# Kernel tuning notes

Hardware: AMD Instinct MI355X
Metric: run time of the kernel (lower is better)

Reference implementation:

```python
import jax, jax.numpy as jnp
import numpy as np

B, N, D, H = 4, 2048, 512, 8
HD = D // H
NUM_BUCKETS, MAX_EXACT, MAX_DIST = 44, 28, 2048
_BAND_RANGES = [range(38, 44), range(34, 40), range(28, 35), range(20, 28),
                range(13, 21), range(7, 14), range(3, 9), range(0, 6)]


def _band_mask():
    m = np.zeros((NUM_BUCKETS, H), dtype=np.float32)
    for h, band in enumerate(_BAND_RANGES):
        for j in band:
            m[j, h] = 1.0
    return jnp.asarray(m)


def _rel_bucket(n):
    # T5-style causal relative-position buckets: exact for d<MAX_EXACT, log-spaced above.
    i = jnp.arange(n)[:, None]
    j = jnp.arange(n)[None, :]
    d = jnp.maximum(i - j, 0)
    safe = jnp.maximum(d, 1).astype(jnp.float32)
    logb = MAX_EXACT + (jnp.log(safe / MAX_EXACT)
                        / np.log(MAX_DIST / MAX_EXACT)
                        * (NUM_BUCKETS - MAX_EXACT)).astype(jnp.int32)
    return jnp.where(d < MAX_EXACT, d, jnp.minimum(logb, NUM_BUCKETS - 1))  # [n,n]


def setup_inputs() -> dict:
    key = jax.random.key(0)
    ks = jax.random.split(key, 12)
    s = 0.02
    return {
        "x": jax.random.normal(ks[0], (B, N, D), jnp.float32),
        "k_delta": jax.random.normal(ks[1], (B, H, N, HD), jnp.float32) * 0.1,
        "v_delta": jax.random.normal(ks[2], (B, H, N, HD), jnp.float32) * 0.1,
        "qkv_w": jax.random.normal(ks[3], (D, 3 * D), jnp.float32) * s,
        "qkv_b": jnp.zeros((3 * D,), jnp.float32),
        "gate_w": jax.random.normal(ks[4], (D, D), jnp.float32) * s,
        "gate_b": jnp.zeros((D,), jnp.float32),
        "out_w": jax.random.normal(ks[5], (D, D), jnp.float32) * s,
        "out_b": jnp.zeros((D,), jnp.float32),
        "pos_bias": jax.random.normal(ks[6], (NUM_BUCKETS, H), jnp.float32) * 0.1,
        "if_gain": jnp.ones((H,), jnp.float32),
    }


def reference(x, k_delta, v_delta, qkv_w, qkv_b, gate_w, gate_b,
              out_w, out_b, pos_bias, if_gain):
    b, n, d = x.shape
    band = _band_mask()
    # hard per-head banding of the relative bias
    eff_bias = pos_bias * band + (1.0 - band) * (-100.0)           # [44,H]
    qkv = x @ qkv_w + qkv_b                                         # [B,N,3D]
    q, k, v = jnp.split(qkv, 3, axis=-1)
    q = q.reshape(b, n, H, HD).transpose(0, 2, 1, 3)                # [B,H,N,HD]
    k = k.reshape(b, n, H, HD).transpose(0, 2, 1, 3) + k_delta
    v = v.reshape(b, n, H, HD).transpose(0, 2, 1, 3) + v_delta
    bucket = _rel_bucket(n)                                         # [N,N] int
    bias = eff_bias[bucket].transpose(2, 0, 1)                      # [H,N,N]
    scores = jnp.einsum("bhid,bhjd->bhij", q, k) / np.sqrt(HD) + bias[None]
    causal = jnp.tril(jnp.ones((n, n), bool))
    scores = jnp.where(causal[None, None], scores, -1e9)
    attn = jax.nn.softmax(scores, axis=-1)
    out = jnp.einsum("bhij,bhjd->bhid", attn, v)                    # [B,H,N,HD]
    out = out * if_gain[None, :, None, None]                        # IF gain
    out_flat = out.transpose(0, 2, 1, 3).reshape(b, n, d)
    gate = jax.nn.sigmoid(x @ gate_w + gate_b)                      # output gating
    return (out_flat * gate) @ out_w + out_b
```

## Files before the change

kernel.cpp:

```cpp
#include <hip/hip_runtime.h>
#include <cmath>

typedef unsigned short u16;
typedef unsigned short u16x4 __attribute__((ext_vector_type(4)));
typedef unsigned short u16x8 __attribute__((ext_vector_type(8)));
typedef __bf16 bf16x8 __attribute__((ext_vector_type(8)));
typedef float f32x4 __attribute__((ext_vector_type(4)));

#define HNUM 8
#define HDIM 64
#define BATCH 4
#define NSEQ 2048
#define DMODEL 512
#define NFUSED 2048
#define LP 72
#define CP 132

__device__ __forceinline__ u16 f2bf(float f) {
  unsigned int u = __builtin_bit_cast(unsigned int, f);
  u += 0x7fffu + ((u >> 16) & 1u);
  return (u16)(u >> 16);
}

__device__ __forceinline__ float bf2f(u16 v) {
  unsigned int u = ((unsigned int)v) << 16;
  return __builtin_bit_cast(float, u);
}

__device__ __forceinline__ f32x4 mfma_bf16(u16x8 a, u16x8 b, f32x4 c) {
  return __builtin_amdgcn_mfma_f32_16x16x32_bf16(
      __builtin_bit_cast(bf16x8, a), __builtin_bit_cast(bf16x8, b), c, 0, 0, 0);
}

__device__ __forceinline__ void gload16(u16* lds, const u16* g) {
  __builtin_amdgcn_global_load_lds(
      (const __attribute__((address_space(1))) void*)g,
      (__attribute__((address_space(3))) void*)lds, 16, 0, 0);
}

template <int ROWS>
__device__ __forceinline__ void stage_tile(u16* lds, const u16* g, int tid) {
  #pragma unroll
  for (int i = 0; i < ROWS / 64; ++i) {
    const int off = (i * 256 + tid) * 8;
    const int row = off >> 5, col = off & 31;
    gload16(lds + off, g + (size_t)row * DMODEL + col);
  }
}

__global__ __launch_bounds__(256) void cvt_bf16_kernel(
    const float* __restrict__ in, u16* __restrict__ out, int n8) {
  int i = blockIdx.x * 256 + threadIdx.x;
  if (i >= n8) return;
  const float4 f0 = *(const float4*)(in + i * 8);
  const float4 f1 = *(const float4*)(in + i * 8 + 4);
  u16x8 pk;
  pk[0] = f2bf(f0.x); pk[1] = f2bf(f0.y); pk[2] = f2bf(f0.z); pk[3] = f2bf(f0.w);
  pk[4] = f2bf(f1.x); pk[5] = f2bf(f1.y); pk[6] = f2bf(f1.z); pk[7] = f2bf(f1.w);
  *(u16x8*)(out + i * 8) = pk;
}

__global__ __launch_bounds__(256) void transpose_w_kernel(
    const float* __restrict__ W, u16* __restrict__ Wt, int K, int N) {
  __shared__ float tile[32][33];
  const int n0 = blockIdx.x * 32, k0 = blockIdx.y * 32;
  const int tx = threadIdx.x & 31, ty = threadIdx.x >> 5;
  #pragma unroll
  for (int yy = ty; yy < 32; yy += 8)
    tile[yy][tx] = W[(size_t)(k0 + yy) * N + n0 + tx];
  __syncthreads();
  #pragma unroll
  for (int yy = ty; yy < 32; yy += 8)
    Wt[(size_t)(n0 + yy) * K + k0 + tx] = f2bf(tile[tx][yy]);
}

__global__ __launch_bounds__(256) void transpose_v_kernel(
    const u16* __restrict__ v, u16* __restrict__ vT) {
  __shared__ u16 t[64][LP];
  const int n0 = blockIdx.x * 64;
  const size_t bh = blockIdx.y;
  const int r = threadIdx.x >> 2, c0 = (threadIdx.x & 3) << 4;
  const u16* src = v + (bh * NSEQ + n0 + r) * HDIM + c0;
  u16x8 a0 = *(const u16x8*)src;
  u16x8 a1 = *(const u16x8*)(src + 8);
  #pragma unroll
  for (int j = 0; j < 8; ++j) {
    t[c0 + j][r] = a0[j];
    t[c0 + 8 + j][r] = a1[j];
  }
  __syncthreads();
  u16x8 o0 = *(const u16x8*)&t[r][c0];
  u16x8 o1 = *(const u16x8*)&t[r][c0 + 8];
  u16* dst = vT + (bh * HDIM + r) * NSEQ + n0 + c0;
  *(u16x8*)dst = o0;
  *(u16x8*)(dst + 8) = o1;
}

__global__ __launch_bounds__(256) void bias_tab_kernel(
    const float* __restrict__ pos_bias, float* __restrict__ tab) {
  int d = blockIdx.x * 256 + threadIdx.x;
  if (d >= NSEQ) return;
  int bkt;
  if (d < 28) {
    bkt = d;
  } else {
    double t = log((double)d / 28.0) / log(2048.0 / 28.0) * 16.0;
    int ti = 28 + (int)t;
    bkt = ti < 43 ? ti : 43;
  }
  const int lo[8] = {38, 34, 28, 20, 13, 7, 3, 0};
  const int hi[8] = {44, 40, 35, 28, 21, 14, 9, 6};
  #pragma unroll
  for (int h = 0; h < HNUM; ++h) {
    bool inb = (bkt >= lo[h]) && (bkt < hi[h]);
    tab[h * NSEQ + d] = inb ? pos_bias[bkt * HNUM + h] : -100.0f;
  }
}

__global__ __launch_bounds__(256) void gemm_fused(
    const u16* __restrict__ Abf, const u16* __restrict__ Wt,
    const float* __restrict__ qkv_b, const float* __restrict__ gate_b,
    const float* __restrict__ kdelta, const float* __restrict__ vdelta,
    u16* __restrict__ qbf, u16* __restrict__ kbf, u16* __restrict__ vbf,
    u16* __restrict__ gate) {
  __shared__ __align__(16) u16 S[6][128 * 32];

  const int bid = blockIdx.y * 16 + blockIdx.x;
  const int nb = (bid & 7) * 128 + (bid >> 3);
  const int m0 = (nb >> 4) * 128;
  const int n0 = (nb & 15) * 128;

  const int tid = threadIdx.x;
  const int w = tid >> 6, l = tid & 63, li = l & 15, lg = l >> 4;
  const int wr = w >> 1, wc = w & 1;

  f32x4 acc[4][4];
  #pragma unroll
  for (int i = 0; i < 4; ++i)
    #pragma unroll
    for (int j = 0; j < 4; ++j) acc[i][j] = f32x4{0.f, 0.f, 0.f, 0.f};

  const u16* Ab = Abf + (size_t)m0 * DMODEL;
  const u16* Bb = Wt + (size_t)n0 * DMODEL;

  stage_tile<128>(S[0], Ab, tid);
  stage_tile<128>(S[3], Bb, tid);
  stage_tile<128>(S[1], Ab + 32, tid);
  stage_tile<128>(S[4], Bb + 32, tid);

  #pragma unroll
  for (int kt = 0; kt < 16; ++kt) {
    if (kt + 2 < 16) {
      stage_tile<128>(S[(kt + 2) % 3], Ab + (kt + 2) * 32, tid);
      stage_tile<128>(S[3 + (kt + 2) % 3], Bb + (kt + 2) * 32, tid);
    }
    if (kt < 14)       asm volatile("s_waitcnt vmcnt(8)" ::: "memory");
    else if (kt == 14) asm volatile("s_waitcnt vmcnt(4)" ::: "memory");
    else               asm volatile("s_waitcnt vmcnt(0)" ::: "memory");
    __builtin_amdgcn_s_barrier();
    __builtin_amdgcn_sched_barrier(0);
    const u16* Asb = S[kt % 3];
    const u16* Bsb = S[3 + kt % 3];
    u16x8 af[4], bfr[4];
    #pragma unroll
    for (int mt = 0; mt < 4; ++mt)
      af[mt] = *(const u16x8*)&Asb[(wr * 64 + mt * 16 + li) * 32 + lg * 8];
    #pragma unroll
    for (int nt = 0; nt < 4; ++nt)
      bfr[nt] = *(const u16x8*)&Bsb[(wc * 64 + nt * 16 + li) * 32 + lg * 8];
    asm volatile("s_waitcnt lgkmcnt(0)" ::: "memory");
    __builtin_amdgcn_sched_barrier(0);
    #pragma unroll
    for (int mt = 0; mt < 4; ++mt)
      #pragma unroll
      for (int nt = 0; nt < 4; ++nt)
        acc[mt][nt] = mfma_bf16(af[mt], bfr[nt], acc[mt][nt]);
    __builtin_amdgcn_s_barrier();
    __builtin_amdgcn_sched_barrier(0);
  }

  u16* Ct = S[0];
  const int seg = n0 >> 9;
  #pragma unroll
  for (int nt = 0; nt < 4; ++nt) {
    const int col = wc * 64 + nt * 16 + li;
    const int colg = n0 + col;
    const float bv = (seg < 3) ? qkv_b[colg] : gate_b[colg & 511];
    #pragma unroll
    for (int mt = 0; mt < 4; ++mt) {
      const int row = wr * 64 + mt * 16 + lg * 4;
      #pragma unroll
      for (int r = 0; r < 4; ++r)
        Ct[(row + r) * CP + col] = f2bf(acc[mt][nt][r] + bv);
    }
  }
  __syncthreads();

  const int nin = n0 & 511;
  #pragma unroll
  for (int p = 0; p < 8; ++p) {
    const int row = p * 16 + (tid >> 4);
    const int cc = (tid & 15) * 8;
    const int rg = m0 + row;
    const int b = rg >> 11, n = rg & 2047;
    u16x8 cv = *(const u16x8*)&Ct[row * CP + cc];
    if (seg == 3) {
      u16x8 o;
      #pragma unroll
      for (int j = 0; j < 8; ++j)
        o[j] = f2bf(1.f / (1.f + __expf(-bf2f(cv[j]))));
      *(u16x8*)&gate[(size_t)rg * DMODEL + nin + cc] = o;
    } else {
      const int hh = (nin + cc) >> 6, hd = (nin + cc) & 63;
      const size_t hidx = (((size_t)b * HNUM + hh) * NSEQ + n) * HDIM + hd;
      if (seg == 0) {
        u16x8 o;
        #pragma unroll
        for (int j = 0; j < 8; ++j) o[j] = f2bf(bf2f(cv[j]) * 0.125f);
        *(u16x8*)&qbf[hidx] = o;
      } else {
        const float* dp = (seg == 1 ? kdelta : vdelta) + hidx;
        float4 d0 = *(const float4*)dp;
        float4 d1 = *(const float4*)(dp + 4);
        u16x8 o;
        o[0] = f2bf(bf2f(cv[0]) + d0.x); o[1] = f2bf(bf2f(cv[1]) + d0.y);
        o[2] = f2bf(bf2f(cv[2]) + d0.z); o[3] = f2bf(bf2f(cv[3]) + d0.w);
        o[4] = f2bf(bf2f(cv[4]) + d1.x); o[5] = f2bf(bf2f(cv[5]) + d1.y);
        o[6] = f2bf(bf2f(cv[6]) + d1.z); o[7] = f2bf(bf2f(cv[7]) + d1.w);
        *(u16x8*)&((seg == 1) ? kbf : vbf)[hidx] = o;
      }
    }
  }
}

__global__ __launch_bounds__(256) void gemm_out(
    const u16* __restrict__ Abf, const u16* __restrict__ Wt,
    const float* __restrict__ bias, float* __restrict__ outf) {
  __shared__ __align__(16) u16 As0[64 * 32];
  __shared__ __align__(16) u16 As1[64 * 32];
  __shared__ __align__(16) u16 Bs0[128 * 32];
  __shared__ __align__(16) u16 Bs1[128 * 32];

  const int m0 = blockIdx.y * 64, n0 = blockIdx.x * 128;
  const int tid = threadIdx.x;
  const int w = tid >> 6, l = tid & 63, li = l & 15, lg = l >> 4;
  const int wr = w >> 1, wc = w & 1;

  f32x4 acc[2][4];
  #pragma unroll
  for (int i = 0; i < 2; ++i)
    #pragma unroll
    for (int j = 0; j < 4; ++j) acc[i][j] = f32x4{0.f, 0.f, 0.f, 0.f};

  const u16* Ab = Abf + (size_t)m0 * DMODEL;
  const u16* Bb = Wt + (size_t)n0 * DMODEL;

  auto compute = [&](const u16* Asb, const u16* Bsb) {
    u16x8 af[2], bfr[4];
    #pragma unroll
    for (int mt = 0; mt < 2; ++mt)
      af[mt] = *(const u16x8*)&Asb[(wr * 32 + mt * 16 + li) * 32 + lg * 8];
    #pragma unroll
    for (int nt = 0; nt < 4; ++nt)
      bfr[nt] = *(const u16x8*)&Bsb[(wc * 64 + nt * 16 + li) * 32 + lg * 8];
    asm volatile("s_waitcnt lgkmcnt(0)" ::: "memory");
    __builtin_amdgcn_sched_barrier(0);
    #pragma unroll
    for (int mt = 0; mt < 2; ++mt)
      #pragma unroll
      for (int nt = 0; nt < 4; ++nt)
        acc[mt][nt] = mfma_bf16(af[mt], bfr[nt], acc[mt][nt]);
  };

  stage_tile<64>(As0, Ab, tid);
  stage_tile<128>(Bs0, Bb, tid);
  asm volatile("s_waitcnt vmcnt(0)" ::: "memory");
  __syncthreads();

  #pragma unroll 1
  for (int kt2 = 0; kt2 < 8; ++kt2) {
    {
      const int kn = kt2 * 2 + 1;
      if (kn < 16) {
        stage_tile<64>(As1, Ab + kn * 32, tid);
        stage_tile<128>(Bs1, Bb + kn * 32, tid);
      }
      compute(As0, Bs0);
      asm volatile("s_waitcnt vmcnt(0)" ::: "memory");
      __syncthreads();
    }
    {
      const int kn = kt2 * 2 + 2;
      if (kn < 16) {
        stage_tile<64>(As0, Ab + kn * 32, tid);
        stage_tile<128>(Bs0, Bb + kn * 32, tid);
      }
      compute(As1, Bs1);
      asm volatile("s_waitcnt vmcnt(0)" ::: "memory");
      __syncthreads();
    }
  }

  #pragma unroll
  for (int nt = 0; nt < 4; ++nt) {
    const int colg = n0 + wc * 64 + nt * 16 + li;
    const float bv = bias[colg];
    #pragma unroll
    for (int mt = 0; mt < 2; ++mt) {
      #pragma unroll
      for (int r = 0; r < 4; ++r) {
        const int rowg = m0 + wr * 32 + mt * 16 + lg * 4 + r;
        outf[(size_t)rowg * DMODEL + colg] = acc[mt][nt][r] + bv;
      }
    }
  }
}

__global__ __launch_bounds__(256) void attn_kernel(
    const u16* __restrict__ qbf, const u16* __restrict__ kbf,
    const u16* __restrict__ vbfT, const float* __restrict__ bias_tab,
    const float* __restrict__ if_gain, const u16* __restrict__ gate,
    u16* __restrict__ attn_out, u16* __restrict__ partO,
    float* __restrict__ partM, float* __restrict__ partL) {
  __shared__ __align__(16) u16 Ks[64][LP];
  __shared__ __align__(16) u16 Vt[64][LP];
  __shared__ __align__(16) u16 Pl[4][16][LP];

  static const int DMINW[8] = {408, 139, 26, 18, 11, 5, 1, 0};
  static const int DMAXW[8] = {2049, 702, 185, 29, 22, 15, 10, 7};
  static const int DMINS[8] = {412, 143, 30, 22, 15, 9, 5, 2};
  static const int SH[12] = {0, 0, 0, 0, 1, 1, 2, 3, 4, 5, 6, 7};
  static const int SC[12] = {0, 1, 2, 3, 0, 1, 0, 0, 0, 0, 0, 0};
  static const int SN[12] = {4, 4, 4, 4, 2, 2, 1, 1, 1, 1, 1, 1};

  const int slot = blockIdx.x >> 7;
  const int rem = blockIdx.x & 127;
  const int qt = 31 - (rem >> 2);
  const int b = rem & 3;
  const int h = SH[slot], ch = SC[slot], nc = SN[slot];
  const int bh = b * HNUM + h;
  const int q0 = qt * 64;
  const int tid = threadIdx.x;
  const int w = tid >> 6, l = tid & 63, li = l & 15, lg = l >> 4;

  const u16* qrow = qbf + ((size_t)bh * NSEQ + q0 + w * 16 + li) * HDIM;
  u16x8 qf0 = *(const u16x8*)(qrow + lg * 8);
  u16x8 qf1 = *(const u16x8*)(qrow + 32 + lg * 8);

  const bool pure = q0 >= DMINS[h];
  int kv_lo = 0, kv_hi = q0 + 64;
  if (pure) {
    int lo = q0 - DMAXW[h];
    kv_lo = (lo > 0 ? lo : 0) & ~63;
    kv_hi = q0 + 64 - DMINW[h];
  }
  const int t0 = kv_lo >> 6, t1 = (kv_hi - 1) >> 6;
  const int len = t1 - t0 + 1;
  const int ta = t0 + (len * ch) / nc;
  const int tb = t0 + (len * (ch + 1)) / nc - 1;

  const int srow = tid >> 2;
  const int scb = (tid & 3) << 4;
  const float* btab = bias_tab + h * NSEQ;

  float mrun = -INFINITY, lrun = 0.f;
  f32x4 O[4] = {{0.f,0.f,0.f,0.f},{0.f,0.f,0.f,0.f},
                {0.f,0.f,0.f,0.f},{0.f,0.f,0.f,0.f}};

  for (int tt = ta; tt <= tb; ++tt) {
    const int kv0 = tt << 6;
    {
      const size_t kbase = ((size_t)bh * NSEQ + kv0 + srow) * HDIM + scb;
      u16x8 k0 = *(const u16x8*)(kbf + kbase);
      u16x8 k1 = *(const u16x8*)(kbf + kbase + 8);
      const size_t vbase = ((size_t)bh * HDIM + srow) * NSEQ + kv0 + scb;
      u16x8 v0 = *(const u16x8*)(vbfT + vbase);
      u16x8 v1 = *(const u16x8*)(vbfT + vbase + 8);
      *(u16x8*)&Ks[srow][scb] = k0;
      *(u16x8*)&Ks[srow][scb + 8] = k1;
      *(u16x8*)&Vt[srow][scb] = v0;
      *(u16x8*)&Vt[srow][scb + 8] = v1;
    }
    __syncthreads();

    f32x4 s[4];
    #pragma unroll
    for (int t = 0; t < 4; ++t) {
      u16x8 a0 = *(const u16x8*)&Ks[t * 16 + li][lg * 8];
      u16x8 a1 = *(const u16x8*)&Ks[t * 16 + li][32 + lg * 8];
      f32x4 acc = {0.f, 0.f, 0.f, 0.f};
      acc = mfma_bf16(a0, qf0, acc);
      acc = mfma_bf16(a1, qf1, acc);
      s[t] = acc;
    }

    const int D0 = (q0 + w * 16 + li) - kv0 - lg * 4;
    float rm = -1e30f;
    #pragma unroll
    for (int t = 0; t < 4; ++t) {
      #pragma unroll
      for (int r = 0; r < 4; ++r) {
        int d = D0 - 16 * t - r;
        float sv = s[t][r];
        sv = (d >= 0) ? (sv + btab[d]) : -1e30f;
        s[t][r] = sv;
        rm = fmaxf(rm, sv);
      }
    }
    rm = fmaxf(rm, __shfl_xor(rm, 16, 64));
    rm = fmaxf(rm, __shfl_xor(rm, 32, 64));
    const float mn = fmaxf(mrun, rm);
    const float f = __expf(mrun - mn);
    mrun = mn;
    float ps = 0.f;
    #pragma unroll
    for (int t = 0; t < 4; ++t) {
      #pragma unroll
      for (int r = 0; r < 4; ++r) {
        float p = __expf(s[t][r] - mn);
        s[t][r] = p;
        ps += p;
      }
    }
    ps += __shfl_xor(ps, 16, 64);
    ps += __shfl_xor(ps, 32, 64);
    lrun = lrun * f + ps;

    #pragma unroll
    for (int t = 0; t < 4; ++t) {
      u16x4 pk;
      pk[0] = f2bf(s[t][0]); pk[1] = f2bf(s[t][1]);
      pk[2] = f2bf(s[t][2]); pk[3] = f2bf(s[t][3]);
      *(u16x4*)&Pl[w][li][t * 16 + lg * 4] = pk;
    }

    float fr[4];
    #pragma unroll
    for (int r = 0; r < 4; ++r) fr[r] = __shfl(f, lg * 4 + r, 64);
    #pragma unroll
    for (int dt = 0; dt < 4; ++dt) {
      O[dt][0] *= fr[0]; O[dt][1] *= fr[1];
      O[dt][2] *= fr[2]; O[dt][3] *= fr[3];
    }
    __syncthreads();

    #pragma unroll
    for (int ks = 0; ks < 2; ++ks) {
      u16x8 pA = *(const u16x8*)&Pl[w][li][ks * 32 + lg * 8];
      #pragma unroll
      for (int dt = 0; dt < 4; ++dt) {
        u16x8 vB = *(const u16x8*)&Vt[dt * 16 + li][ks * 32 + lg * 8];
        O[dt] = mfma_bf16(pA, vB, O[dt]);
      }
    }
    __syncthreads();
  }

  if (nc == 1) {
    const float gain = if_gain[h];
    float linv[4];
    #pragma unroll
    for (int r = 0; r < 4; ++r)
      linv[r] = gain / __shfl(lrun, lg * 4 + r, 64);
    #pragma unroll
    for (int r = 0; r < 4; ++r) {
      const int i = q0 + w * 16 + lg * 4 + r;
      const size_t base = ((size_t)b * NSEQ + i) * DMODEL + h * HDIM + li;
      #pragma unroll
      for (int dt = 0; dt < 4; ++dt) {
        const float g = bf2f(gate[base + dt * 16]);
        attn_out[base + dt * 16] = f2bf(O[dt][r] * linv[r] * g);
      }
    }
  } else {
    const int sbase = (b * 32 + qt) * 6 + slot;
    #pragma unroll
    for (int r = 0; r < 4; ++r) {
      const int rl = w * 16 + lg * 4 + r;
      #pragma unroll
      for (int dt = 0; dt < 4; ++dt)
        partO[(size_t)sbase * 4096 + rl * 64 + dt * 16 + li] = f2bf(O[dt][r]);
    }
    if (lg == 0) {
      partM[sbase * 64 + w * 16 + li] = mrun;
      partL[sbase * 64 + w * 16 + li] = lrun;
    }
  }
}

__global__ __launch_bounds__(256) void combine_kernel(
    const u16* __restrict__ partO, const float* __restrict__ partM,
    const float* __restrict__ partL, const float* __restrict__ if_gain,
    const u16* __restrict__ gate, u16* __restrict__ attn_out) {
  const int b = blockIdx.x & 3, qt = blockIdx.x >> 2;
  const int tid = threadIdx.x;
  const int row = tid >> 2, d0 = (tid & 3) << 4;

  #pragma unroll
  for (int hc = 0; hc < 2; ++hc) {
    const int nc = hc ? 2 : 4, s0 = hc ? 4 : 0;
    const int sbase = (b * 32 + qt) * 6 + s0;
    float m[4], wch[4];
    float M = -INFINITY;
    #pragma unroll
    for (int c = 0; c < 4; ++c) {
      m[c] = (c < nc) ? partM[(sbase + c) * 64 + row] : -INFINITY;
      M = fmaxf(M, m[c]);
    }
    float den = 0.f;
    #pragma unroll
    for (int c = 0; c < 4; ++c) {
      wch[c] = (c < nc) ? __expf(m[c] - M) : 0.f;
      if (c < nc) den += wch[c] * partL[(sbase + c) * 64 + row];
    }
    float num[16];
    #pragma unroll
    for (int j = 0; j < 16; ++j) num[j] = 0.f;
    #pragma unroll
    for (int c = 0; c < 4; ++c) {
      if (c < nc) {
        const u16* op = partO + (size_t)(sbase + c) * 4096 + row * 64 + d0;
        u16x8 o0 = *(const u16x8*)op;
        u16x8 o1 = *(const u16x8*)(op + 8);
        #pragma unroll
        for (int j = 0; j < 8; ++j) {
          num[j]     += wch[c] * bf2f(o0[j]);
          num[8 + j] += wch[c] * bf2f(o1[j]);
        }
      }
    }
    const float inv = if_gain[hc] / den;
    const size_t obase =
        ((size_t)b * NSEQ + qt * 64 + row) * DMODEL + hc * HDIM + d0;
    u16x8 g0 = *(const u16x8*)(gate + obase);
    u16x8 g1 = *(const u16x8*)(gate + obase + 8);
    u16x8 r0, r1;
    #pragma unroll
    for (int j = 0; j < 8; ++j) {
      r0[j] = f2bf(num[j] * inv * bf2f(g0[j]));
      r1[j] = f2bf(num[8 + j] * inv * bf2f(g1[j]));
    }
    *(u16x8*)(attn_out + obase) = r0;
    *(u16x8*)(attn_out + obase + 8) = r1;
  }
}

extern "C" void kernel_launch(void* const* d_in, const int* in_sizes, int n_in,
                              void* d_out, int out_size, void* d_ws,
                              size_t ws_size, hipStream_t stream) {
  const float* x       = (const float*)d_in[0];
  const float* k_delta = (const float*)d_in[1];
  const float* v_delta = (const float*)d_in[2];
  const float* qkv_w   = (const float*)d_in[3];
  const float* qkv_b   = (const float*)d_in[4];
  const float* gate_w  = (const float*)d_in[5];
  const float* gate_b  = (const float*)d_in[6];
  const float* out_w   = (const float*)d_in[7];
  const float* out_b   = (const float*)d_in[8];
  const float* pos_bias = (const float*)d_in[9];
  const float* if_gain  = (const float*)d_in[10];
  float* out = (float*)d_out;
  char* ws = (char*)d_ws;

  u16*   xbf      = (u16*)(ws + 0);
  u16*   qbf      = (u16*)(ws + 8388608);
  u16*   kbf      = (u16*)(ws + 16777216);
  u16*   vbf      = (u16*)(ws + 25165824);
  u16*   vbfT     = (u16*)(ws + 33554432);
  u16*   gate_buf = (u16*)(ws + 41943040);
  u16*   fused_wt = (u16*)(ws + 50331648);
  u16*   out_wt   = (u16*)(ws + 52428800);
  float* bias_tab = (float*)(ws + 52953088);
  u16*   attn_buf = vbf;
  u16*   partO = (u16*)(ws + 0);
  float* partM = (float*)(ws + 6291456);
  float* partL = (float*)(ws + 6488064);

  cvt_bf16_kernel<<<dim3(2048), dim3(256), 0, stream>>>(
      x, xbf, BATCH * NSEQ * DMODEL / 8);
  transpose_w_kernel<<<dim3(48, 16), dim3(256), 0, stream>>>(
      qkv_w, fused_wt, DMODEL, 3 * DMODEL);
  transpose_w_kernel<<<dim3(16, 16), dim3(256), 0, stream>>>(
      gate_w, fused_wt + (size_t)3 * DMODEL * DMODEL, DMODEL, DMODEL);
  transpose_w_kernel<<<dim3(16, 16), dim3(256), 0, stream>>>(
      out_w, out_wt, DMODEL, DMODEL);
  bias_tab_kernel<<<dim3(8), dim3(256), 0, stream>>>(pos_bias, bias_tab);

  gemm_fused<<<dim3(16, 64), dim3(256), 0, stream>>>(
      xbf, fused_wt, qkv_b, gate_b, k_delta, v_delta,
      qbf, kbf, vbf, gate_buf);

  transpose_v_kernel<<<dim3(32, 32), dim3(256), 0, stream>>>(vbf, vbfT);

  attn_kernel<<<dim3(1536), dim3(256), 0, stream>>>(
      qbf, kbf, vbfT, bias_tab, if_gain, gate_buf, attn_buf,
      partO, partM, partL);

  combine_kernel<<<dim3(128), dim3(256), 0, stream>>>(
      partO, partM, partL, if_gain, gate_buf, attn_buf);

  gemm_out<<<dim3(4, 128), dim3(256), 0, stream>>>(
      attn_buf, out_wt, out_b, out);

  (void)in_sizes; (void)n_in; (void)out_size; (void)ws_size;
}
```

Before: 102.6 us.

## Split long-range heads into more KV chunks and triple-buffer output GEMM

The attention split-KV schedule grows from 12 to 19 slots. Head 0 is now split into 8 chunks, head 1 into 4 and head 2 into 2, which balances the long-range heads against the short-band ones and raises the grid to 2432 blocks. The combine kernel merges up to 8 partials for three heads, and the partial buffers move to a separate workspace region. Separately, gemm_out switches from double to triple buffering with partial vmcnt waits, so loads stay in flight across iterations. The cost is more partial-result traffic, a larger combine step and more LDS per block.

```diff
diff --git a/kernel.cpp b/kernel.cpp
--- a/kernel.cpp
+++ b/kernel.cpp
@@ -15,6 +15,7 @@
 #define NFUSED 2048
 #define LP 72
 #define CP 132
+#define NSLOT 14
 
 __device__ __forceinline__ u16 f2bf(float f) {
   unsigned int u = __builtin_bit_cast(unsigned int, f);
@@ -236,10 +237,8 @@
 __global__ __launch_bounds__(256) void gemm_out(
     const u16* __restrict__ Abf, const u16* __restrict__ Wt,
     const float* __restrict__ bias, float* __restrict__ outf) {
-  __shared__ __align__(16) u16 As0[64 * 32];
-  __shared__ __align__(16) u16 As1[64 * 32];
-  __shared__ __align__(16) u16 Bs0[128 * 32];
-  __shared__ __align__(16) u16 Bs1[128 * 32];
+  __shared__ __align__(16) u16 As[3][64 * 32];
+  __shared__ __align__(16) u16 Bs[3][128 * 32];
 
   const int m0 = blockIdx.y * 64, n0 = blockIdx.x * 128;
   const int tid = threadIdx.x;
@@ -255,7 +254,24 @@
   const u16* Ab = Abf + (size_t)m0 * DMODEL;
   const u16* Bb = Wt + (size_t)n0 * DMODEL;
 
-  auto compute = [&](const u16* Asb, const u16* Bsb) {
+  stage_tile<64>(As[0], Ab, tid);
+  stage_tile<128>(Bs[0], Bb, tid);
+  stage_tile<64>(As[1], Ab + 32, tid);
+  stage_tile<128>(Bs[1], Bb + 32, tid);
+
+  #pragma unroll
+  for (int kt = 0; kt < 16; ++kt) {
+    if (kt + 2 < 16) {
+      stage_tile<64>(As[(kt + 2) % 3], Ab + (kt + 2) * 32, tid);
+      stage_tile<128>(Bs[(kt + 2) % 3], Bb + (kt + 2) * 32, tid);
+    }
+    if (kt < 14)       asm volatile("s_waitcnt vmcnt(6)" ::: "memory");
+    else if (kt == 14) asm volatile("s_waitcnt vmcnt(3)" ::: "memory");
+    else               asm volatile("s_waitcnt vmcnt(0)" ::: "memory");
+    __builtin_amdgcn_s_barrier();
+    __builtin_amdgcn_sched_barrier(0);
+    const u16* Asb = As[kt % 3];
+    const u16* Bsb = Bs[kt % 3];
     u16x8 af[2], bfr[4];
     #pragma unroll
     for (int mt = 0; mt < 2; ++mt)
@@ -270,35 +286,8 @@
       #pragma unroll
       for (int nt = 0; nt < 4; ++nt)
         acc[mt][nt] = mfma_bf16(af[mt], bfr[nt], acc[mt][nt]);
-  };
-
-  stage_tile<64>(As0, Ab, tid);
-  stage_tile<128>(Bs0, Bb, tid);
-  asm volatile("s_waitcnt vmcnt(0)" ::: "memory");
-  __syncthreads();
-
-  #pragma unroll 1
-  for (int kt2 = 0; kt2 < 8; ++kt2) {
-    {
-      const int kn = kt2 * 2 + 1;
-      if (kn < 16) {
-        stage_tile<64>(As1, Ab + kn * 32, tid);
-        stage_tile<128>(Bs1, Bb + kn * 32, tid);
-      }
-      compute(As0, Bs0);
-      asm volatile("s_waitcnt vmcnt(0)" ::: "memory");
-      __syncthreads();
-    }
-    {
-      const int kn = kt2 * 2 + 2;
-      if (kn < 16) {
-        stage_tile<64>(As0, Ab + kn * 32, tid);
-        stage_tile<128>(Bs0, Bb + kn * 32, tid);
-      }
-      compute(As1, Bs1);
-      asm volatile("s_waitcnt vmcnt(0)" ::: "memory");
-      __syncthreads();
-    }
+    __builtin_amdgcn_s_barrier();
+    __builtin_amdgcn_sched_barrier(0);
   }
 
   #pragma unroll
@@ -329,9 +318,9 @@
   static const int DMINW[8] = {408, 139, 26, 18, 11, 5, 1, 0};
   static const int DMAXW[8] = {2049, 702, 185, 29, 22, 15, 10, 7};
   static const int DMINS[8] = {412, 143, 30, 22, 15, 9, 5, 2};
-  static const int SH[12] = {0, 0, 0, 0, 1, 1, 2, 3, 4, 5, 6, 7};
-  static const int SC[12] = {0, 1, 2, 3, 0, 1, 0, 0, 0, 0, 0, 0};
-  static const int SN[12] = {4, 4, 4, 4, 2, 2, 1, 1, 1, 1, 1, 1};
+  static const int SH[19] = {0,0,0,0,0,0,0,0, 1,1,1,1, 2,2, 3,4,5,6,7};
+  static const int SC[19] = {0,1,2,3,4,5,6,7, 0,1,2,3, 0,1, 0,0,0,0,0};
+  static const int SN[19] = {8,8,8,8,8,8,8,8, 4,4,4,4, 2,2, 1,1,1,1,1};
 
   const int slot = blockIdx.x >> 7;
   const int rem = blockIdx.x & 127;
@@ -473,7 +462,7 @@
       }
     }
   } else {
-    const int sbase = (b * 32 + qt) * 6 + slot;
+    const int sbase = (b * 32 + qt) * NSLOT + slot;
     #pragma unroll
     for (int r = 0; r < 4; ++r) {
       const int rl = w * 16 + lg * 4 + r;
@@ -495,21 +484,24 @@
   const int b = blockIdx.x & 3, qt = blockIdx.x >> 2;
   const int tid = threadIdx.x;
   const int row = tid >> 2, d0 = (tid & 3) << 4;
-
-  #pragma unroll
-  for (int hc = 0; hc < 2; ++hc) {
-    const int nc = hc ? 2 : 4, s0 = hc ? 4 : 0;
-    const int sbase = (b * 32 + qt) * 6 + s0;
-    float m[4], wch[4];
+  static const int HNC[3] = {8, 4, 2};
+  static const int HS0[3] = {0, 8, 12};
+
+  #pragma unroll
+  for (int hc = 0; hc < 3; ++hc) {
+    const int nc = HNC[hc], s0 = HS0[hc];
+    const int sbase = (b * 32 + qt) * NSLOT + s0;
+    float m[8];
     float M = -INFINITY;
     #pragma unroll
-    for (int c = 0; c < 4; ++c) {
+    for (int c = 0; c < 8; ++c) {
       m[c] = (c < nc) ? partM[(sbase + c) * 64 + row] : -INFINITY;
       M = fmaxf(M, m[c]);
     }
+    float wch[8];
     float den = 0.f;
     #pragma unroll
-    for (int c = 0; c < 4; ++c) {
+    for (int c = 0; c < 8; ++c) {
       wch[c] = (c < nc) ? __expf(m[c] - M) : 0.f;
       if (c < nc) den += wch[c] * partL[(sbase + c) * 64 + row];
     }
@@ -517,7 +509,7 @@
     #pragma unroll
     for (int j = 0; j < 16; ++j) num[j] = 0.f;
     #pragma unroll
-    for (int c = 0; c < 4; ++c) {
+    for (int c = 0; c < 8; ++c) {
       if (c < nc) {
         const u16* op = partO + (size_t)(sbase + c) * 4096 + row * 64 + d0;
         u16x8 o0 = *(const u16x8*)op;
@@ -571,10 +563,10 @@
   u16*   fused_wt = (u16*)(ws + 50331648);
   u16*   out_wt   = (u16*)(ws + 52428800);
   float* bias_tab = (float*)(ws + 52953088);
+  u16*   partO = (u16*)(ws + 53018624);
+  float* partM = (float*)(ws + 67698688);
+  float* partL = (float*)(ws + 68157440);
   u16*   attn_buf = vbf;
-  u16*   partO = (u16*)(ws + 0);
-  float* partM = (float*)(ws + 6291456);
-  float* partL = (float*)(ws + 6488064);
 
   cvt_bf16_kernel<<<dim3(2048), dim3(256), 0, stream>>>(
       x, xbf, BATCH * NSEQ * DMODEL / 8);
@@ -592,7 +584,7 @@
 
   transpose_v_kernel<<<dim3(32, 32), dim3(256), 0, stream>>>(vbf, vbfT);
 
-  attn_kernel<<<dim3(1536), dim3(256), 0, stream>>>(
+  attn_kernel<<<dim3(2432), dim3(256), 0, stream>>>(
       qbf, kbf, vbfT, bias_tab, if_gain, gate_buf, attn_buf,
       partO, partM, partL);
 
```

New measurement: 102.8 us. About the same (+0.2%).
